# Kernel optimization log

Measured on AMD Instinct MI355X. Metric: run time of the kernel, lower is better.

Reference implementation:

```python
import jax, jax.numpy as jnp
import numpy as np

N_PTS = 250000
N_VOX = 60000
D_PT = 256
D_VOX = 256
MID = 256
NUM_CLASS = 20
BN_EPS = 1e-5


def _batchnorm(x, gamma, beta):
    # torch BatchNorm1d in train mode: batch mean / biased variance over dim 0
    mean = jnp.mean(x, axis=0)
    var = jnp.var(x, axis=0)
    return gamma * (x - mean) * jax.lax.rsqrt(var + BN_EPS) + beta


def setup_inputs() -> dict:
    key = jax.random.key(0)
    ks = jax.random.split(key, 8)
    point_feature = jax.random.normal(ks[0], (N_PTS, D_PT), dtype=jnp.float32)
    voxel_feature = jax.random.normal(ks[1], (N_VOX, D_VOX), dtype=jnp.float32)
    p2vmap = jax.random.randint(ks[2], (N_PTS,), 0, N_VOX, dtype=jnp.int64)
    voxel_logits = jax.random.normal(ks[3], (N_VOX, NUM_CLASS), dtype=jnp.float32)
    W1 = jax.random.normal(ks[4], (MID, D_PT + D_VOX), dtype=jnp.float32) * 0.02
    b1 = jnp.zeros((MID,), dtype=jnp.float32)
    W2 = jax.random.normal(ks[5], (MID, D_VOX), dtype=jnp.float32) * 0.02
    b2 = jnp.zeros((MID,), dtype=jnp.float32)
    g1 = jnp.ones((MID,), dtype=jnp.float32)
    be1 = jnp.zeros((MID,), dtype=jnp.float32)
    g2 = jnp.ones((MID,), dtype=jnp.float32)
    be2 = jnp.zeros((MID,), dtype=jnp.float32)
    return {"point_feature": point_feature, "voxel_feature": voxel_feature,
            "voxel_logits": voxel_logits, "W1": W1, "b1": b1, "g1": g1, "be1": be1,
            "W2": W2, "b2": b2, "g2": g2, "be2": be2, "p2vmap": p2vmap}


def reference(point_feature, voxel_feature, voxel_logits, W1, b1, g1, be1,
              W2, b2, g2, be2, p2vmap):
    # gather voxel feature to each point: [N_pts, D_VOX]
    unet_point_feature = voxel_feature[p2vmap]
    x = jnp.concatenate([point_feature, unet_point_feature], axis=1)  # [N_pts, 512]
    x = jax.nn.relu(_batchnorm(x @ W1.T + b1, g1, be1))               # [N_pts, MID]
    cls_prob = jax.nn.softmax(voxel_logits, axis=1)                   # [N_vox, C]
    cls_fea = jnp.einsum('bc,bf->cf', cls_prob, voxel_feature)        # [C, D_VOX]
    cls_fea = _batchnorm(cls_fea @ W2.T + b2, g2, be2)                # [C, MID]
    seg_logits = x @ cls_fea.T                                        # [N_pts, C]
    return seg_logits
```

## Files before the change

### kernel.cpp

```cpp
#include <hip/hip_runtime.h>
#include <hip/hip_bf16.h>

#define N_PTS 250000
#define N_VOX 60000
#define MID   256
#define KDIM  512
#define NCLS  20
#define BN_EPS 1e-5f

typedef __attribute__((ext_vector_type(8))) short short8;
typedef __attribute__((ext_vector_type(4))) float f32x4;

__device__ __forceinline__ unsigned short f2bf(float f) {
    unsigned u = __builtin_bit_cast(unsigned, f);
    u += 0x7FFFu + ((u >> 16) & 1u);
    return (unsigned short)(u >> 16);
}
__device__ __forceinline__ float bf2f(unsigned short h) {
    unsigned u = ((unsigned)h) << 16;
    return __builtin_bit_cast(float, u);
}

__global__ __launch_bounds__(256) void gemm1_kernel(
    const float* __restrict__ point, const float* __restrict__ vox,
    const float* __restrict__ W1, const float* __restrict__ b1,
    const int* __restrict__ p2v,
    unsigned short* __restrict__ hbuf,
    float* __restrict__ colsum, float* __restrict__ colsumsq)
{
    __shared__ unsigned short As[128 * 40];
    __shared__ unsigned short Bs[128 * 40];

    const int tid = threadIdx.x;
    const int bN = blockIdx.x;
    const int bM = blockIdx.y;
    const int r0  = tid >> 3;
    const int off = tid & 7;

    int rA[4]; int vm[4]; int rB[4];
    #pragma unroll
    for (int i = 0; i < 4; ++i) {
        int rg = bM * 128 + r0 + 32 * i;
        if (rg > N_PTS - 1) rg = N_PTS - 1;
        rA[i] = rg;
        vm[i] = p2v[rg];
        rB[i] = bN * 128 + r0 + 32 * i;
    }

    f32x4 zero4 = {0.f, 0.f, 0.f, 0.f};
    f32x4 acc[4][4];
    #pragma unroll
    for (int mi = 0; mi < 4; ++mi)
        #pragma unroll
        for (int ni = 0; ni < 4; ++ni)
            acc[mi][ni] = zero4;

    const int lane = tid & 63;
    const int wv = tid >> 6;
    const int wm = wv & 1;
    const int wn = wv >> 1;
    const int l15 = lane & 15;
    const int l4  = lane >> 4;

    for (int kt = 0; kt < 16; ++kt) {
        const int kOff = (kt & 7) * 32 + off * 4;
        #pragma unroll
        for (int i = 0; i < 4; ++i) {
            const float* src = (kt < 8)
                ? (point + (size_t)rA[i] * 256 + kOff)
                : (vox   + (size_t)vm[i] * 256 + kOff);
            const float4 v = *(const float4*)src;
            unsigned lo = (unsigned)f2bf(v.x) | ((unsigned)f2bf(v.y) << 16);
            unsigned hi = (unsigned)f2bf(v.z) | ((unsigned)f2bf(v.w) << 16);
            *(uint2*)&As[(r0 + 32 * i) * 40 + off * 4] = make_uint2(lo, hi);

            const float* srcB = W1 + (size_t)rB[i] * 512 + kt * 32 + off * 4;
            const float4 w = *(const float4*)srcB;
            unsigned lo2 = (unsigned)f2bf(w.x) | ((unsigned)f2bf(w.y) << 16);
            unsigned hi2 = (unsigned)f2bf(w.z) | ((unsigned)f2bf(w.w) << 16);
            *(uint2*)&Bs[(r0 + 32 * i) * 40 + off * 4] = make_uint2(lo2, hi2);
        }
        __syncthreads();

        short8 a[4], b[4];
        #pragma unroll
        for (int mi = 0; mi < 4; ++mi)
            a[mi] = *(const short8*)&As[(wm * 64 + mi * 16 + l15) * 40 + l4 * 8];
        #pragma unroll
        for (int ni = 0; ni < 4; ++ni)
            b[ni] = *(const short8*)&Bs[(wn * 64 + ni * 16 + l15) * 40 + l4 * 8];
        #pragma unroll
        for (int mi = 0; mi < 4; ++mi)
            #pragma unroll
            for (int ni = 0; ni < 4; ++ni)
                acc[mi][ni] = __builtin_amdgcn_mfma_f32_16x16x32_bf16(
                                  a[mi], b[ni], acc[mi][ni], 0, 0, 0);
        __syncthreads();
    }

    #pragma unroll
    for (int ni = 0; ni < 4; ++ni) {
        const int colG = bN * 128 + wn * 64 + ni * 16 + l15;
        const float b1v = b1[colG];
        float s = 0.f, sq = 0.f;
        #pragma unroll
        for (int mi = 0; mi < 4; ++mi) {
            const int rgBase = bM * 128 + wm * 64 + mi * 16 + l4 * 4;
            #pragma unroll
            for (int r = 0; r < 4; ++r) {
                const int rr = rgBase + r;
                if (rr < N_PTS) {
                    const float hv = acc[mi][ni][r] + b1v;
                    hbuf[(size_t)rr * 256 + colG] = f2bf(hv);
                    s  += hv;
                    sq += hv * hv;
                }
            }
        }
        s  += __shfl_xor(s, 16);  s  += __shfl_xor(s, 32);
        sq += __shfl_xor(sq, 16); sq += __shfl_xor(sq, 32);
        if (lane < 16) {
            atomicAdd(&colsum[colG], s);
            atomicAdd(&colsumsq[colG], sq);
        }
    }
}

__global__ __launch_bounds__(256) void stats_kernel(
    const float* __restrict__ colsum, const float* __restrict__ colsumsq,
    const float* __restrict__ g1, const float* __restrict__ be1,
    float* __restrict__ scl, float* __restrict__ shf)
{
    const int j = threadIdx.x;
    const float mean = colsum[j] * (1.0f / N_PTS);
    const float var  = colsumsq[j] * (1.0f / N_PTS) - mean * mean;
    const float sc = g1[j] * rsqrtf(var + BN_EPS);
    scl[j] = sc;
    shf[j] = be1[j] - mean * sc;
}

#define NCHUNK 938
__global__ __launch_bounds__(256) void cls_acc_kernel(
    const float* __restrict__ logits, const float* __restrict__ vox,
    float* __restrict__ cls_acc)
{
    __shared__ float probs[64 * 24];
    const int tid = threadIdx.x;
    float acc[NCLS];
    #pragma unroll
    for (int c = 0; c < NCLS; ++c) acc[c] = 0.f;

    for (int ci = 0; ci < 4; ++ci) {
        const int chunk = blockIdx.x * 4 + ci;
        if (chunk >= NCHUNK) break;
        const int v0 = chunk * 64;
        __syncthreads();
        if (tid < 64) {
            const int v = v0 + tid;
            if (v < N_VOX) {
                float l[NCLS];
                float mx = -1e30f;
                #pragma unroll
                for (int c = 0; c < NCLS; ++c) {
                    l[c] = logits[(size_t)v * NCLS + c];
                    mx = fmaxf(mx, l[c]);
                }
                float sum = 0.f;
                #pragma unroll
                for (int c = 0; c < NCLS; ++c) { l[c] = __expf(l[c] - mx); sum += l[c]; }
                const float inv = 1.f / sum;
                #pragma unroll
                for (int c = 0; c < NCLS; ++c) probs[tid * 24 + c] = l[c] * inv;
            }
        }
        __syncthreads();
        const int nb = min(64, N_VOX - v0);
        for (int b = 0; b < nb; ++b) {
            const float vv = vox[(size_t)(v0 + b) * 256 + tid];
            #pragma unroll
            for (int c4 = 0; c4 < 5; ++c4) {
                const float4 p = *(const float4*)&probs[b * 24 + c4 * 4];
                acc[c4 * 4 + 0] += p.x * vv;
                acc[c4 * 4 + 1] += p.y * vv;
                acc[c4 * 4 + 2] += p.z * vv;
                acc[c4 * 4 + 3] += p.w * vv;
            }
        }
    }
    #pragma unroll
    for (int c = 0; c < NCLS; ++c)
        atomicAdd(&cls_acc[c * 256 + tid], acc[c]);
}

__global__ __launch_bounds__(256) void cls_fea2_kernel(
    const float* __restrict__ cls_acc, const float* __restrict__ W2,
    const float* __restrict__ b2, const float* __restrict__ g2,
    const float* __restrict__ be2, float* __restrict__ cls_fin)
{
    __shared__ float cf[NCLS * 256];
    const int tid = threadIdx.x;
    for (int i = tid; i < NCLS * 256; i += 256) cf[i] = cls_acc[i];
    __syncthreads();

    float acc[NCLS];
    #pragma unroll
    for (int c = 0; c < NCLS; ++c) acc[c] = b2[tid];
    for (int k = 0; k < 256; k += 4) {
        const float4 w = *(const float4*)&W2[(size_t)tid * 256 + k];
        #pragma unroll
        for (int c = 0; c < NCLS; ++c) {
            const float4 f = *(const float4*)&cf[c * 256 + k];
            acc[c] += w.x * f.x + w.y * f.y + w.z * f.z + w.w * f.w;
        }
    }
    float mean = 0.f;
    #pragma unroll
    for (int c = 0; c < NCLS; ++c) mean += acc[c];
    mean *= (1.f / NCLS);
    float var = 0.f;
    #pragma unroll
    for (int c = 0; c < NCLS; ++c) { const float d = acc[c] - mean; var += d * d; }
    var *= (1.f / NCLS);
    const float sc = g2[tid] * rsqrtf(var + BN_EPS);
    const float bb = be2[tid];
    #pragma unroll
    for (int c = 0; c < NCLS; ++c)
        cls_fin[c * 256 + tid] = (acc[c] - mean) * sc + bb;
}

__global__ __launch_bounds__(256) void gemm2_kernel(
    const unsigned short* __restrict__ hbuf,
    const float* __restrict__ scl, const float* __restrict__ shf,
    const float* __restrict__ cls_fin,
    float* __restrict__ out)
{
    __shared__ unsigned short xs[64 * 258];
    __shared__ float cls[NCLS * 256];

    const int tid = threadIdx.x;
    for (int i = tid; i < NCLS * 256; i += 256) cls[i] = cls_fin[i];

    const int rb = blockIdx.x * 64;
    const int rwave = tid >> 6;
    const int c4 = tid & 63;
    const float4 sc4 = *(const float4*)&scl[c4 * 4];
    const float4 sh4 = *(const float4*)&shf[c4 * 4];

    #pragma unroll
    for (int i = 0; i < 16; ++i) {
        const int row = rwave + i * 4;
        const int rg = rb + row;
        ushort4 hv = make_ushort4(0, 0, 0, 0);
        if (rg < N_PTS) hv = *(const ushort4*)&hbuf[(size_t)rg * 256 + c4 * 4];
        const float x0 = fmaxf(bf2f(hv.x) * sc4.x + sh4.x, 0.f);
        const float x1 = fmaxf(bf2f(hv.y) * sc4.y + sh4.y, 0.f);
        const float x2 = fmaxf(bf2f(hv.z) * sc4.z + sh4.z, 0.f);
        const float x3 = fmaxf(bf2f(hv.w) * sc4.w + sh4.w, 0.f);
        ushort4 xv = make_ushort4(f2bf(x0), f2bf(x1), f2bf(x2), f2bf(x3));
        *(ushort4*)&xs[row * 258 + c4 * 4] = xv;
    }
    __syncthreads();

    const int r = tid & 63;
    const int g = tid >> 6;
    float a[5] = {0.f, 0.f, 0.f, 0.f, 0.f};
    const float* cb = &cls[g * 5 * 256];
    for (int k = 0; k < 256; k += 2) {
        const unsigned xp = *(const unsigned*)&xs[r * 258 + k];
        const float x0 = bf2f((unsigned short)(xp & 0xFFFFu));
        const float x1 = bf2f((unsigned short)(xp >> 16));
        #pragma unroll
        for (int j = 0; j < 5; ++j) {
            const float2 cv = *(const float2*)&cb[j * 256 + k];
            a[j] += x0 * cv.x + x1 * cv.y;
        }
    }
    const int rg = rb + r;
    if (rg < N_PTS) {
        float* o = &out[(size_t)rg * 20 + g * 5];
        #pragma unroll
        for (int j = 0; j < 5; ++j) o[j] = a[j];
    }
}

extern "C" void kernel_launch(void* const* d_in, const int* in_sizes, int n_in,
                              void* d_out, int out_size, void* d_ws, size_t ws_size,
                              hipStream_t stream)
{
    const float* point  = (const float*)d_in[0];
    const float* vox    = (const float*)d_in[1];
    const float* logits = (const float*)d_in[2];
    const float* W1     = (const float*)d_in[3];
    const float* b1     = (const float*)d_in[4];
    const float* g1     = (const float*)d_in[5];
    const float* be1    = (const float*)d_in[6];
    const float* W2     = (const float*)d_in[7];
    const float* b2     = (const float*)d_in[8];
    const float* g2     = (const float*)d_in[9];
    const float* be2    = (const float*)d_in[10];
    const int*   p2v    = (const int*)d_in[11];
    float* out = (float*)d_out;

    char* ws = (char*)d_ws;
    unsigned short* hbuf = (unsigned short*)ws;
    size_t o = (size_t)N_PTS * 256 * 2;
    float* colsum   = (float*)(ws + o); o += 1024;
    float* colsumsq = (float*)(ws + o); o += 1024;
    float* scl      = (float*)(ws + o); o += 1024;
    float* shf      = (float*)(ws + o); o += 1024;
    float* cls_acc  = (float*)(ws + o); o += (size_t)NCLS * 256 * 4;
    float* cls_fin  = (float*)(ws + o); o += (size_t)NCLS * 256 * 4;

    hipMemsetAsync(colsum, 0, 2 * 1024, stream);
    hipMemsetAsync(cls_acc, 0, (size_t)NCLS * 256 * 4, stream);

    gemm1_kernel<<<dim3(2, 1954), 256, 0, stream>>>(point, vox, W1, b1, p2v,
                                                    hbuf, colsum, colsumsq);
    cls_acc_kernel<<<235, 256, 0, stream>>>(logits, vox, cls_acc);
    stats_kernel<<<1, 256, 0, stream>>>(colsum, colsumsq, g1, be1, scl, shf);
    cls_fea2_kernel<<<1, 256, 0, stream>>>(cls_acc, W2, b2, g2, be2, cls_fin);
    gemm2_kernel<<<3907, 256, 0, stream>>>(hbuf, scl, shf, cls_fin, out);
}
```

Baseline: 792.7 us.

## Restructure both GEMMs with async LDS loads, pre-packed weights, and MFMA gemm2

```diff
diff --git a/kernel.cpp b/kernel.cpp
--- a/kernel.cpp
+++ b/kernel.cpp
@@ -10,51 +10,56 @@
 
 typedef __attribute__((ext_vector_type(8))) short short8;
 typedef __attribute__((ext_vector_type(4))) float f32x4;
-
-__device__ __forceinline__ unsigned short f2bf(float f) {
-    unsigned u = __builtin_bit_cast(unsigned, f);
+typedef unsigned int u32;
+
+__device__ __forceinline__ unsigned short f2bf_rne(float f) {
+    u32 u = __builtin_bit_cast(u32, f);
     u += 0x7FFFu + ((u >> 16) & 1u);
     return (unsigned short)(u >> 16);
 }
-__device__ __forceinline__ float bf2f(unsigned short h) {
-    unsigned u = ((unsigned)h) << 16;
-    return __builtin_bit_cast(float, u);
-}
-
-__global__ __launch_bounds__(256) void gemm1_kernel(
+__device__ __forceinline__ u32 pack2_rnd(float lo, float hi) {
+    u32 a = __builtin_bit_cast(u32, lo) + 0x8000u;
+    u32 b = __builtin_bit_cast(u32, hi) + 0x8000u;
+    return __builtin_amdgcn_perm(b, a, 0x07060302);
+}
+__device__ __forceinline__ float bfLo(u32 w) { return __builtin_bit_cast(float, w << 16); }
+__device__ __forceinline__ float bfHi(u32 w) { return __builtin_bit_cast(float, w & 0xFFFF0000u); }
+
+__device__ __forceinline__ void async_copy16(void* lds, const void* g) {
+    __builtin_amdgcn_global_load_lds(
+        (const __attribute__((address_space(1))) u32*)g,
+        (__attribute__((address_space(3))) u32*)lds, 16, 0, 0);
+}
+
+__global__ __launch_bounds__(256) void prep_w1_kernel(
+    const float* __restrict__ W1, unsigned short* __restrict__ W1s)
+{
+    const int idx = blockIdx.x * 256 + threadIdx.x;
+    const int lane = idx & 63;
+    const int ni = (idx >> 6) & 15;
+    const int kt = idx >> 10;
+    const int n = ni * 16 + (lane & 15);
+    const int k = kt * 32 + (lane >> 4) * 8;
+    const float* src = W1 + (size_t)n * 512 + k;
+    unsigned short v[8];
+    #pragma unroll
+    for (int j = 0; j < 8; ++j) v[j] = f2bf_rne(src[j]);
+    ushort4* dst = (ushort4*)(W1s + (size_t)idx * 8);
+    dst[0] = make_ushort4(v[0], v[1], v[2], v[3]);
+    dst[1] = make_ushort4(v[4], v[5], v[6], v[7]);
+}
+
+__global__ __launch_bounds__(256, 2) void gemm1_kernel(
     const float* __restrict__ point, const float* __restrict__ vox,
-    const float* __restrict__ W1, const float* __restrict__ b1,
+    const unsigned short* __restrict__ W1s, const float* __restrict__ b1,
     const int* __restrict__ p2v,
     unsigned short* __restrict__ hbuf,
     float* __restrict__ colsum, float* __restrict__ colsumsq)
 {
-    __shared__ unsigned short As[128 * 40];
-    __shared__ unsigned short Bs[128 * 40];
+    __shared__ float As[2][128 * 32];
 
     const int tid = threadIdx.x;
-    const int bN = blockIdx.x;
-    const int bM = blockIdx.y;
-    const int r0  = tid >> 3;
-    const int off = tid & 7;
-
-    int rA[4]; int vm[4]; int rB[4];
-    #pragma unroll
-    for (int i = 0; i < 4; ++i) {
-        int rg = bM * 128 + r0 + 32 * i;
-        if (rg > N_PTS - 1) rg = N_PTS - 1;
-        rA[i] = rg;
-        vm[i] = p2v[rg];
-        rB[i] = bN * 128 + r0 + 32 * i;
-    }
-
-    f32x4 zero4 = {0.f, 0.f, 0.f, 0.f};
-    f32x4 acc[4][4];
-    #pragma unroll
-    for (int mi = 0; mi < 4; ++mi)
-        #pragma unroll
-        for (int ni = 0; ni < 4; ++ni)
-            acc[mi][ni] = zero4;
-
+    const int bM = blockIdx.x;
     const int lane = tid & 63;
     const int wv = tid >> 6;
     const int wm = wv & 1;
@@ -62,45 +67,81 @@
     const int l15 = lane & 15;
     const int l4  = lane >> 4;
 
+    const float* aP[4];
+    const float* aV[4];
+    #pragma unroll
+    for (int l = 0; l < 4; ++l) {
+        const int idx = l * 256 + tid;
+        const int r = idx >> 3;
+        const int c = (idx & 7) ^ (r & 7);
+        int rg = bM * 128 + r;
+        if (rg > N_PTS - 1) rg = N_PTS - 1;
+        const int vm = p2v[rg];
+        aP[l] = point + (size_t)rg * 256 + c * 4;
+        aV[l] = vox   + (size_t)vm * 256 + c * 4;
+    }
+
+    f32x4 acc[4][8];
+    #pragma unroll
+    for (int mi = 0; mi < 4; ++mi)
+        #pragma unroll
+        for (int j = 0; j < 8; ++j)
+            acc[mi][j] = (f32x4){0.f, 0.f, 0.f, 0.f};
+
+    #pragma unroll
+    for (int l = 0; l < 4; ++l)
+        async_copy16(&As[0][(l * 256 + tid) * 4], aP[l]);
+
+    #pragma unroll 2
     for (int kt = 0; kt < 16; ++kt) {
-        const int kOff = (kt & 7) * 32 + off * 4;
-        #pragma unroll
-        for (int i = 0; i < 4; ++i) {
-            const float* src = (kt < 8)
-                ? (point + (size_t)rA[i] * 256 + kOff)
-                : (vox   + (size_t)vm[i] * 256 + kOff);
-            const float4 v = *(const float4*)src;
-            unsigned lo = (unsigned)f2bf(v.x) | ((unsigned)f2bf(v.y) << 16);
-            unsigned hi = (unsigned)f2bf(v.z) | ((unsigned)f2bf(v.w) << 16);
-            *(uint2*)&As[(r0 + 32 * i) * 40 + off * 4] = make_uint2(lo, hi);
-
-            const float* srcB = W1 + (size_t)rB[i] * 512 + kt * 32 + off * 4;
-            const float4 w = *(const float4*)srcB;
-            unsigned lo2 = (unsigned)f2bf(w.x) | ((unsigned)f2bf(w.y) << 16);
-            unsigned hi2 = (unsigned)f2bf(w.z) | ((unsigned)f2bf(w.w) << 16);
-            *(uint2*)&Bs[(r0 + 32 * i) * 40 + off * 4] = make_uint2(lo2, hi2);
-        }
         __syncthreads();
 
-        short8 a[4], b[4];
+        short8 bfr[8];
+        #pragma unroll
+        for (int j = 0; j < 8; ++j) {
+            const int ni = wn * 8 + j;
+            bfr[j] = *(const short8*)(W1s + ((size_t)(kt * 16 + ni) * 64 + lane) * 8);
+        }
+
+        if (kt < 15) {
+            const int kn = kt + 1;
+            const int ko = (kn & 7) * 32;
+            #pragma unroll
+            for (int l = 0; l < 4; ++l) {
+                const float* src = (kn < 8) ? (aP[l] + ko) : (aV[l] + ko);
+                async_copy16(&As[(kn & 1)][(l * 256 + tid) * 4], src);
+            }
+        }
+
+        const float* buf = As[kt & 1];
+        short8 afr[4];
+        #pragma unroll
+        for (int mi = 0; mi < 4; ++mi) {
+            const int m = wm * 64 + mi * 16 + l15;
+            const int c0 = (l4 * 2) ^ (m & 7);
+            const float* base = buf + m * 32;
+            const f32x4 v0 = *(const f32x4*)(base + c0 * 4);
+            const f32x4 v1 = *(const f32x4*)(base + (c0 ^ 1) * 4);
+            u32 q[4];
+            q[0] = pack2_rnd(v0[0], v0[1]);
+            q[1] = pack2_rnd(v0[2], v0[3]);
+            q[2] = pack2_rnd(v1[0], v1[1]);
+            q[3] = pack2_rnd(v1[2], v1[3]);
+            u32* ap = (u32*)&afr[mi];
+            ap[0] = q[0]; ap[1] = q[1]; ap[2] = q[2]; ap[3] = q[3];
+        }
+
         #pragma unroll
         for (int mi = 0; mi < 4; ++mi)
-            a[mi] = *(const short8*)&As[(wm * 64 + mi * 16 + l15) * 40 + l4 * 8];
-        #pragma unroll
-        for (int ni = 0; ni < 4; ++ni)
-            b[ni] = *(const short8*)&Bs[(wn * 64 + ni * 16 + l15) * 40 + l4 * 8];
-        #pragma unroll
-        for (int mi = 0; mi < 4; ++mi)
-            #pragma unroll
-            for (int ni = 0; ni < 4; ++ni)
-                acc[mi][ni] = __builtin_amdgcn_mfma_f32_16x16x32_bf16(
-                                  a[mi], b[ni], acc[mi][ni], 0, 0, 0);
-        __syncthreads();
-    }
-
-    #pragma unroll
-    for (int ni = 0; ni < 4; ++ni) {
-        const int colG = bN * 128 + wn * 64 + ni * 16 + l15;
+            #pragma unroll
+            for (int j = 0; j < 8; ++j)
+                acc[mi][j] = __builtin_amdgcn_mfma_f32_16x16x32_bf16(
+                                 afr[mi], bfr[j], acc[mi][j], 0, 0, 0);
+    }
+
+    #pragma unroll
+    for (int j = 0; j < 8; ++j) {
+        const int colG = wn * 128 + j * 16 + l15;
         const float b1v = b1[colG];
         float s = 0.f, sq = 0.f;
         #pragma unroll
@@ -110,8 +151,8 @@
             for (int r = 0; r < 4; ++r) {
                 const int rr = rgBase + r;
                 if (rr < N_PTS) {
-                    const float hv = acc[mi][ni][r] + b1v;
-                    hbuf[(size_t)rr * 256 + colG] = f2bf(hv);
+                    const float hv = acc[mi][j][r] + b1v;
+                    hbuf[(size_t)rr * 256 + colG] = f2bf_rne(hv);
                     s  += hv;
                     sq += hv * hv;
                 }
@@ -124,19 +165,6 @@
             atomicAdd(&colsumsq[colG], sq);
         }
     }
-}
-
-__global__ __launch_bounds__(256) void stats_kernel(
-    const float* __restrict__ colsum, const float* __restrict__ colsumsq,
-    const float* __restrict__ g1, const float* __restrict__ be1,
-    float* __restrict__ scl, float* __restrict__ shf)
-{
-    const int j = threadIdx.x;
-    const float mean = colsum[j] * (1.0f / N_PTS);
-    const float var  = colsumsq[j] * (1.0f / N_PTS) - mean * mean;
-    const float sc = g1[j] * rsqrtf(var + BN_EPS);
-    scl[j] = sc;
-    shf[j] = be1[j] - mean * sc;
 }
 
 #define NCHUNK 938
@@ -192,13 +220,26 @@
         atomicAdd(&cls_acc[c * 256 + tid], acc[c]);
 }
 
-__global__ __launch_bounds__(256) void cls_fea2_kernel(
+__global__ __launch_bounds__(256) void fuse_kernel(
+    const float* __restrict__ colsum, const float* __restrict__ colsumsq,
+    const float* __restrict__ g1, const float* __restrict__ be1,
+    float* __restrict__ scl, float* __restrict__ shf,
     const float* __restrict__ cls_acc, const float* __restrict__ W2,
     const float* __restrict__ b2, const float* __restrict__ g2,
-    const float* __restrict__ be2, float* __restrict__ cls_fin)
+    const float* __restrict__ be2, unsigned short* __restrict__ cls_frag)
 {
     __shared__ float cf[NCLS * 256];
+    __shared__ float cf2[NCLS * 256];
     const int tid = threadIdx.x;
+
+    {
+        const float mean = colsum[tid] * (1.0f / N_PTS);
+        const float var  = colsumsq[tid] * (1.0f / N_PTS) - mean * mean;
+        const float sc = g1[tid] * rsqrtf(var + BN_EPS);
+        scl[tid] = sc;
+        shf[tid] = be1[tid] - mean * sc;
+    }
+
     for (int i = tid; i < NCLS * 256; i += 256) cf[i] = cls_acc[i];
     __syncthreads();
 
@@ -225,61 +266,95 @@
     const float bb = be2[tid];
     #pragma unroll
     for (int c = 0; c < NCLS; ++c)
-        cls_fin[c * 256 + tid] = (acc[c] - mean) * sc + bb;
+        cf2[c * 256 + tid] = (acc[c] - mean) * sc + bb;
+    __syncthreads();
+
+    #pragma unroll
+    for (int i = 0; i < 4; ++i) {
+        const int idx = i * 256 + tid;
+        const int lane = idx & 63;
+        const int ni = (idx >> 6) & 1;
+        const int kt = idx >> 7;
+        const int n = ni * 16 + (lane & 15);
+        const int k = kt * 32 + (lane >> 4) * 8;
+        unsigned short v[8];
+        #pragma unroll
+        for (int j = 0; j < 8; ++j)
+            v[j] = (n < NCLS) ? f2bf_rne(cf2[n * 256 + k + j]) : (unsigned short)0;
+        ushort4* dst = (ushort4*)(cls_frag + (size_t)idx * 8);
+        dst[0] = make_ushort4(v[0], v[1], v[2], v[3]);
+        dst[1] = make_ushort4(v[4], v[5], v[6], v[7]);
+    }
 }
 
 __global__ __launch_bounds__(256) void gemm2_kernel(
     const unsigned short* __restrict__ hbuf,
     const float* __restrict__ scl, const float* __restrict__ shf,
-    const float* __restrict__ cls_fin,
+    const unsigned short* __restrict__ cls_frag,
     float* __restrict__ out)
 {
-    __shared__ unsigned short xs[64 * 258];
-    __shared__ float cls[NCLS * 256];
-
+    __shared__ float sS[256], sT[256];
     const int tid = threadIdx.x;
-    for (int i = tid; i < NCLS * 256; i += 256) cls[i] = cls_fin[i];
-
-    const int rb = blockIdx.x * 64;
-    const int rwave = tid >> 6;
-    const int c4 = tid & 63;
-    const float4 sc4 = *(const float4*)&scl[c4 * 4];
-    const float4 sh4 = *(const float4*)&shf[c4 * 4];
-
-    #pragma unroll
-    for (int i = 0; i < 16; ++i) {
-        const int row = rwave + i * 4;
-        const int rg = rb + row;
-        ushort4 hv = make_ushort4(0, 0, 0, 0);
-        if (rg < N_PTS) hv = *(const ushort4*)&hbuf[(size_t)rg * 256 + c4 * 4];
-        const float x0 = fmaxf(bf2f(hv.x) * sc4.x + sh4.x, 0.f);
-        const float x1 = fmaxf(bf2f(hv.y) * sc4.y + sh4.y, 0.f);
-        const float x2 = fmaxf(bf2f(hv.z) * sc4.z + sh4.z, 0.f);
-        const float x3 = fmaxf(bf2f(hv.w) * sc4.w + sh4.w, 0.f);
-        ushort4 xv = make_ushort4(f2bf(x0), f2bf(x1), f2bf(x2), f2bf(x3));
-        *(ushort4*)&xs[row * 258 + c4 * 4] = xv;
-    }
+    sS[tid] = scl[tid];
+    sT[tid] = shf[tid];
     __syncthreads();
 
-    const int r = tid & 63;
-    const int g = tid >> 6;
-    float a[5] = {0.f, 0.f, 0.f, 0.f, 0.f};
-    const float* cb = &cls[g * 5 * 256];
-    for (int k = 0; k < 256; k += 2) {
-        const unsigned xp = *(const unsigned*)&xs[r * 258 + k];
-        const float x0 = bf2f((unsigned short)(xp & 0xFFFFu));
-        const float x1 = bf2f((unsigned short)(xp >> 16));
-        #pragma unroll
-        for (int j = 0; j < 5; ++j) {
-            const float2 cv = *(const float2*)&cb[j * 256 + k];
-            a[j] += x0 * cv.x + x1 * cv.y;
-        }
-    }
-    const int rg = rb + r;
-    if (rg < N_PTS) {
-        float* o = &out[(size_t)rg * 20 + g * 5];
-        #pragma unroll
-        for (int j = 0; j < 5; ++j) o[j] = a[j];
+    const int lane = tid & 63;
+    const int w = tid >> 6;
+    const int l15 = lane & 15;
+    const int l4 = lane >> 4;
+    const int mBase = blockIdx.x * 256 + w * 64;
+
+    f32x4 acc[4][2];
+    #pragma unroll
+    for (int mi = 0; mi < 4; ++mi) {
+        acc[mi][0] = (f32x4){0.f, 0.f, 0.f, 0.f};
+        acc[mi][1] = (f32x4){0.f, 0.f, 0.f, 0.f};
+    }
+
+    #pragma unroll
+    for (int kt = 0; kt < 8; ++kt) {
+        const int k0 = kt * 32 + l4 * 8;
+        const short8 bf0 = *(const short8*)(cls_frag + ((kt * 2 + 0) * 64 + lane) * 8);
+        const short8 bf1 = *(const short8*)(cls_frag + ((kt * 2 + 1) * 64 + lane) * 8);
+        const f32x4 s0 = *(const f32x4*)&sS[k0];
+        const f32x4 s1 = *(const f32x4*)&sS[k0 + 4];
+        const f32x4 t0 = *(const f32x4*)&sT[k0];
+        const f32x4 t1 = *(const f32x4*)&sT[k0 + 4];
+        const float sv[8] = {s0[0], s0[1], s0[2], s0[3], s1[0], s1[1], s1[2], s1[3]};
+        const float tv[8] = {t0[0], t0[1], t0[2], t0[3], t1[0], t1[1], t1[2], t1[3]};
+
+        #pragma unroll
+        for (int mi = 0; mi < 4; ++mi) {
+            int m = mBase + mi * 16 + l15;
+            if (m > N_PTS - 1) m = N_PTS - 1;
+            const uint4 hx = *(const uint4*)(hbuf + (size_t)m * 256 + k0);
+            const u32 wd[4] = {hx.x, hx.y, hx.z, hx.w};
+            short8 a;
+            u32* ap = (u32*)&a;
+            #pragma unroll
+            for (int p = 0; p < 4; ++p) {
+                const float x0 = fmaxf(fmaf(bfLo(wd[p]), sv[2 * p],     tv[2 * p]),     0.f);
+                const float x1 = fmaxf(fmaf(bfHi(wd[p]), sv[2 * p + 1], tv[2 * p + 1]), 0.f);
+                ap[p] = pack2_rnd(x0, x1);
+            }
+            acc[mi][0] = __builtin_amdgcn_mfma_f32_16x16x32_bf16(a, bf0, acc[mi][0], 0, 0, 0);
+            acc[mi][1] = __builtin_amdgcn_mfma_f32_16x16x32_bf16(a, bf1, acc[mi][1], 0, 0, 0);
+        }
+    }
+
+    #pragma unroll
+    for (int mi = 0; mi < 4; ++mi) {
+        #pragma unroll
+        for (int ni = 0; ni < 2; ++ni) {
+            const int n = ni * 16 + l15;
+            #pragma unroll
+            for (int r = 0; r < 4; ++r) {
+                const int m = mBase + mi * 16 + l4 * 4 + r;
+                if (n < NCLS && m < N_PTS)
+                    out[(size_t)m * 20 + n] = acc[mi][ni][r];
+            }
+        }
     }
 }
 
@@ -309,15 +384,17 @@
     float* scl      = (float*)(ws + o); o += 1024;
     float* shf      = (float*)(ws + o); o += 1024;
     float* cls_acc  = (float*)(ws + o); o += (size_t)NCLS * 256 * 4;
-    float* cls_fin  = (float*)(ws + o); o += (size_t)NCLS * 256 * 4;
+    unsigned short* W1s      = (unsigned short*)(ws + o); o += (size_t)16384 * 8 * 2;
+    unsigned short* cls_frag = (unsigned short*)(ws + o); o += (size_t)1024 * 8 * 2;
 
     hipMemsetAsync(colsum, 0, 2 * 1024, stream);
     hipMemsetAsync(cls_acc, 0, (size_t)NCLS * 256 * 4, stream);
 
-    gemm1_kernel<<<dim3(2, 1954), 256, 0, stream>>>(point, vox, W1, b1, p2v,
-                                                    hbuf, colsum, colsumsq);
+    prep_w1_kernel<<<64, 256, 0, stream>>>(W1, W1s);
+    gemm1_kernel<<<1954, 256, 0, stream>>>(point, vox, W1s, b1, p2v,
+                                           hbuf, colsum, colsumsq);
     cls_acc_kernel<<<235, 256, 0, stream>>>(logits, vox, cls_acc);
-    stats_kernel<<<1, 256, 0, stream>>>(colsum, colsumsq, g1, be1, scl, shf);
-    cls_fea2_kernel<<<1, 256, 0, stream>>>(cls_acc, W2, b2, g2, be2, cls_fin);
-    gemm2_kernel<<<3907, 256, 0, stream>>>(hbuf, scl, shf, cls_fin, out);
-}
+    fuse_kernel<<<1, 256, 0, stream>>>(colsum, colsumsq, g1, be1, scl, shf,
+                                       cls_acc, W2, b2, g2, be2, cls_frag);
+    gemm2_kernel<<<977, 256, 0, stream>>>(hbuf, scl, shf, cls_frag, out);
+}
```

Measured after the change: 669.0 us. 15.6% less time.
